# Kernel tuning notes

Hardware: AMD Instinct MI355X
Metric: run time of the kernel (lower is better)

Reference implementation:

```python
import jax, jax.numpy as jnp
import numpy as np

B, T, D, N, H = 1, 256, 512, 8, 64  # batch, seq, d_model, n_heads, d_head
INIT_STD = 0.02
IGNORE = -1000000.0
DUMMY_LOGIT = -1000.0


def setup_inputs() -> dict:
    key = jax.random.key(0)
    ks = jax.random.split(key, 9)
    std = INIT_STD
    inp = {
        'normalized_resid_pre': jax.random.normal(ks[0], (B, T, D), dtype=jnp.float32),
        'W_K1': jax.random.normal(ks[1], (N, D, H), dtype=jnp.float32) * std,
        'W_K2': jax.random.normal(ks[2], (N, D, H), dtype=jnp.float32) * std,
        'W_Q':  jax.random.normal(ks[3], (N, D, H), dtype=jnp.float32) * std,
        'W_V1': jax.random.normal(ks[4], (N, D, H), dtype=jnp.float32) * std,
        'W_V2': jax.random.normal(ks[5], (N, D, H), dtype=jnp.float32) * std,
        'W_Kq': jax.random.normal(ks[6], (N, H, H, H), dtype=jnp.float32) * std,
        'W_Vq': jax.random.normal(ks[7], (N, H, H, H), dtype=jnp.float32) * std,
        'W_O':  jax.random.normal(ks[8], (N, H, D), dtype=jnp.float32) * std,
        'b_K1': jnp.zeros((N, H), dtype=jnp.float32),
        'b_K2': jnp.zeros((N, H), dtype=jnp.float32),
        'b_Q':  jnp.zeros((N, H), dtype=jnp.float32),
        'b_V1': jnp.zeros((N, H), dtype=jnp.float32),
        'b_V2': jnp.zeros((N, H), dtype=jnp.float32),
        'b_O':  jnp.zeros((D,), dtype=jnp.float32),
    }
    return inp


def _trittention(x, W_K1, W_K2, W_Q, W_V1, W_V2, W_Kq, W_Vq, W_O,
                 b_K1, b_K2, b_Q, b_V1, b_V2, b_O):
    b, t, d = x.shape
    n, _, h = W_Q.shape
    proj = lambda W, bias: jnp.einsum('ndh,bpd->bpnh', W, x) + bias
    k1 = proj(W_K1, b_K1)  # (b, t, n, h)
    k2 = proj(W_K2, b_K2)
    q  = proj(W_Q,  b_Q)
    v1 = proj(W_V1, b_V1)
    v2 = proj(W_V2, b_V2)

    # bilinear value over pairs of positions: (b, n, h, s, t) -> flatten (s t)
    v = jnp.einsum('bsni,btnj,nijh->bnhst', v1, v2, W_Vq)
    v = v.reshape(b, n, h, t * t)

    # cubic scores: (b, n, s, t, r) with s=k1 pos, t=k2 pos, r=query pos
    step1 = jnp.einsum('brnk,nijk->bnrij', q, W_Kq)
    step2 = jnp.einsum('bnrij,btnj->bnrit', step1, k2)
    attn = jnp.einsum('bnrit,bsni->bnstr', step2, k1)

    # causal + ordering mask (order_attn=True, attn_eq=False):
    # masked if s>=r or t>=r or s>=t
    s_idx = jnp.arange(t)[:, None, None]
    t_idx = jnp.arange(t)[None, :, None]
    r_idx = jnp.arange(t)[None, None, :]
    mask = (s_idx >= r_idx) | (t_idx >= r_idx) | (s_idx >= t_idx)
    attn = jnp.where(mask, IGNORE, attn)

    # rearrange 'b n s t r -> b n r (s t)' and scale by d_head
    attn = jnp.transpose(attn, (0, 1, 4, 2, 3)).reshape(b, n, t, t * t) / h

    # causal_attn=True: append dummy logit / zero value slot
    dummy_logit = jnp.full((b, n, t, 1), DUMMY_LOGIT, dtype=attn.dtype)
    attn = jnp.concatenate([attn, dummy_logit], axis=-1)
    dummy_value = jnp.zeros((b, n, h, 1), dtype=v.dtype)
    v = jnp.concatenate([v, dummy_value], axis=-1)

    attn = jax.nn.softmax(attn, axis=-1)
    z = jnp.einsum('bnql,bnhl->bqnh', attn, v)
    out = jnp.einsum('bpnh,nhd->bpd', z, W_O) + b_O  # sum over heads folded in
    return out


def reference(normalized_resid_pre, W_K1, W_K2, W_Q, W_V1, W_V2, W_Kq, W_Vq, W_O,
              b_K1, b_K2, b_Q, b_V1, b_V2, b_O):
    return _trittention(normalized_resid_pre, W_K1, W_K2, W_Q, W_V1, W_V2,
                        W_Kq, W_Vq, W_O, b_K1, b_K2, b_Q, b_V1, b_V2, b_O)
```

## Files before the change

kernel.cpp:

```cpp
#include <hip/hip_runtime.h>
#include <hip/hip_bf16.h>
#include <math.h>

#define TT 256
#define DD 512
#define NN 8
#define HH 64
#define PROJ 131072

typedef __attribute__((ext_vector_type(8))) short short8v;
typedef __attribute__((ext_vector_type(4))) short short4v;
typedef __attribute__((ext_vector_type(4))) float f32x4;

__device__ __forceinline__ short f2bf(float x) {
    __hip_bfloat16 h = __float2bfloat16(x);
    return *reinterpret_cast<short*>(&h);
}

#define LGKM0 asm volatile("s_waitcnt lgkmcnt(0)" ::: "memory")

#define F_NUM  0
#define F_DEN  131072
#define F_END  133120
#define S_PB   0
#define S_XB   655360
#define S_WB   786432
#define S_KQB  2097152
#define S_VQB  4194304
#define S_WOB  6291456
#define S_S1B  6553600
#define S_AB   14942208
#define S_GB   23330816

__global__ __launch_bounds__(256) void prep_kernel(
    const float* __restrict__ x, const float* __restrict__ W_Kq,
    const float* __restrict__ W0, const float* __restrict__ W1,
    const float* __restrict__ W2, const float* __restrict__ W3,
    const float* __restrict__ W4, const float* __restrict__ Vq,
    const float* __restrict__ WO, short* __restrict__ sb, float* __restrict__ fz)
{
    __shared__ float plds[64 * 129];
    int b = blockIdx.x;
    int tid = threadIdx.x;
    if (b < 1024) {
        int i = b * 256 + tid;
        const float4 f0 = *(const float4*)(W_Kq + (size_t)i * 8);
        const float4 f1 = *(const float4*)(W_Kq + (size_t)i * 8 + 4);
        short8v o;
        o[0]=f2bf(f0.x); o[1]=f2bf(f0.y); o[2]=f2bf(f0.z); o[3]=f2bf(f0.w);
        o[4]=f2bf(f1.x); o[5]=f2bf(f1.y); o[6]=f2bf(f1.z); o[7]=f2bf(f1.w);
        *(short8v*)(sb + S_KQB + (size_t)i * 8) = o;
    } else if (b < 1088) {
        int i = (b - 1024) * 256 + tid;
        const float4 f0 = *(const float4*)(x + (size_t)i * 8);
        const float4 f1 = *(const float4*)(x + (size_t)i * 8 + 4);
        short8v o;
        o[0]=f2bf(f0.x); o[1]=f2bf(f0.y); o[2]=f2bf(f0.z); o[3]=f2bf(f0.w);
        o[4]=f2bf(f1.x); o[5]=f2bf(f1.y); o[6]=f2bf(f1.z); o[7]=f2bf(f1.w);
        *(short8v*)(sb + S_XB + (size_t)i * 8) = o;
    } else if (b < 1128) {
        int pn = b - 1088; int p = pn >> 3, n = pn & 7;
        const float* Wp = (p==0)?W0:(p==1)?W1:(p==2)?W2:(p==3)?W3:W4;
        const float* src = Wp + (size_t)n * DD * HH;
        short* dst = sb + S_WB + (size_t)pn * HH * DD;
        for (int d0 = 0; d0 < DD; d0 += 64) {
            __syncthreads();
            for (int it = 0; it < 16; ++it) {
                int m = it * 256 + tid;
                int dl = m >> 6, h = m & 63;
                plds[h * 65 + dl] = src[(size_t)(d0 + dl) * 64 + h];
            }
            __syncthreads();
            int h = tid >> 2, seg = tid & 3;
            short8v o0, o1;
            #pragma unroll
            for (int e = 0; e < 8; ++e) o0[e] = f2bf(plds[h * 65 + seg * 16 + e]);
            #pragma unroll
            for (int e = 0; e < 8; ++e) o1[e] = f2bf(plds[h * 65 + seg * 16 + 8 + e]);
            *(short8v*)(dst + (size_t)h * DD + d0 + seg * 16) = o0;
            *(short8v*)(dst + (size_t)h * DD + d0 + seg * 16 + 8) = o1;
        }
    } else if (b < 1640) {
        int bb = b - 1128; int n = bb >> 6, i = bb & 63;
        const float* src = Vq + (size_t)(n * 64 + i) * 4096;
        for (int it = 0; it < 16; ++it) {
            int m = it * 256 + tid;
            int j = m >> 6, h = m & 63;
            plds[h * 65 + j] = src[(size_t)j * 64 + h];
        }
        __syncthreads();
        int h = tid >> 2, seg = tid & 3;
        short8v o0, o1;
        #pragma unroll
        for (int e = 0; e < 8; ++e) o0[e] = f2bf(plds[h * 65 + seg * 16 + e]);
        #pragma unroll
        for (int e = 0; e < 8; ++e) o1[e] = f2bf(plds[h * 65 + seg * 16 + 8 + e]);
        short* dst = sb + S_VQB + (size_t)n * 262144 + (size_t)h * 4096 + i * 64 + seg * 16;
        *(short8v*)dst = o0;
        *(short8v*)(dst + 8) = o1;
    } else if (b < 1672) {
        int bb = b - 1640; int dc = bb & 7, nhc = bb >> 3;
        for (int it = 0; it < 32; ++it) {
            int m = it * 256 + tid;
            int nhl = m >> 6, dl = m & 63;
            plds[dl * 129 + nhl] = WO[(size_t)(nhc * 128 + nhl) * 512 + dc * 64 + dl];
        }
        __syncthreads();
        for (int it = 0; it < 4; ++it) {
            int m = it * 256 + tid;
            int dl = m >> 4, seg = m & 15;
            short8v o;
            #pragma unroll
            for (int e = 0; e < 8; ++e) o[e] = f2bf(plds[dl * 129 + seg * 8 + e]);
            *(short8v*)(sb + S_WOB + (size_t)(dc * 64 + dl) * 512 + nhc * 128 + seg * 8) = o;
        }
    } else {
        int i = (b - 1672) * 1024 + tid * 4;
        *(float4*)(fz + i) = make_float4(0.f, 0.f, 0.f, 0.f);
    }
}

__global__ __launch_bounds__(512) void proj_kernel(
    const short* __restrict__ xb, const short* __restrict__ Wb,
    const float* __restrict__ bK1, const float* __restrict__ bK2,
    const float* __restrict__ bQ,  const float* __restrict__ bV1,
    const float* __restrict__ bV2, short* __restrict__ Pb) {
    int p = blockIdx.x, n = blockIdx.y, mhalf = blockIdx.z;
    int wv = threadIdx.x >> 6, lane = threadIdx.x & 63, g = lane >> 4, c = lane & 15;
    __shared__ short wlds[64 * 520];
    __shared__ short sbuf[8][16 * 72];
    const short* wsrc = Wb + (size_t)(p * 8 + n) * HH * DD;
    for (int it = 0; it < 8; ++it) {
        int idx = it * 512 + threadIdx.x;
        int h = idx >> 6, seg = idx & 63;
        *(short8v*)(&wlds[h * 520 + seg * 8]) = *(const short8v*)(wsrc + (size_t)h * DD + seg * 8);
    }
    __syncthreads();
    int mt = mhalf * 8 + wv;
    f32x4 acc[4];
    #pragma unroll
    for (int ct = 0; ct < 4; ++ct) acc[ct] = (f32x4){0.f, 0.f, 0.f, 0.f};
    for (int ks = 0; ks < 16; ++ks) {
        short8v a = *(const short8v*)(xb + (size_t)(mt * 16 + c) * DD + ks * 32 + g * 8);
        #pragma unroll
        for (int ct = 0; ct < 4; ++ct) {
            short8v b = *(const short8v*)(&wlds[(ct * 16 + c) * 520 + ks * 32 + g * 8]);
            acc[ct] = __builtin_amdgcn_mfma_f32_16x16x32_bf16(a, b, acc[ct], 0, 0, 0);
        }
    }
    const float* bp = (p == 0) ? bK1 : (p == 1) ? bK2 : (p == 2) ? bQ : (p == 3) ? bV1 : bV2;
    short* sbw = &sbuf[wv][0];
    #pragma unroll
    for (int ct = 0; ct < 4; ++ct) {
        float bias = bp[n * 64 + ct * 16 + c];
        #pragma unroll
        for (int m = 0; m < 4; ++m)
            sbw[(g * 4 + m) * 72 + ct * 16 + c] = f2bf(acc[ct][m] + bias);
    }
    LGKM0;
    int rl = lane & 15, sg = lane >> 4;
    short8v o0 = *(const short8v*)(&sbw[rl * 72 + sg * 16]);
    short8v o1 = *(const short8v*)(&sbw[rl * 72 + sg * 16 + 8]);
    short* dst = Pb + (size_t)p * PROJ + (size_t)(n * 256 + mt * 16 + rl) * 64 + sg * 16;
    *(short8v*)dst = o0;
    *(short8v*)(dst + 8) = o1;
}

__global__ __launch_bounds__(256) void bgemm_kernel(
    const short* __restrict__ A0, const short* __restrict__ B0, short* __restrict__ O0,
    const short* __restrict__ A1, const short* __restrict__ B1, short* __restrict__ O1) {
    int mt = blockIdx.x, n = blockIdx.y, z = blockIdx.z;
    const short* A = (z < 4) ? A0 : A1;
    const short* B = (z < 4) ? B0 : B1;
    short* out = (z < 4) ? O0 : O1;
    int cgq = z & 3;
    int wv = threadIdx.x >> 6, lane = threadIdx.x & 63, g = lane >> 4, c = lane & 15;
    __shared__ short sbuf[4][16 * 72];
    short* sbw = &sbuf[wv][0];
    const short* abase = A + ((size_t)n * 256 + mt * 16 + c) * 64 + g * 8;
    short8v a0 = *(const short8v*)abase;
    short8v a1 = *(const short8v*)(abase + 32);
    for (int cg = cgq * 16 + wv; cg < cgq * 16 + 16; cg += 4) {
        f32x4 acc[4];
        #pragma unroll
        for (int jt = 0; jt < 4; ++jt) acc[jt] = (f32x4){0.f, 0.f, 0.f, 0.f};
        const short* bb = B + ((size_t)n * 4096 + cg * 64) * 64;
        #pragma unroll
        for (int jt = 0; jt < 4; ++jt) {
            short8v b0 = *(const short8v*)(bb + (size_t)(jt * 16 + c) * 64 + g * 8);
            short8v b1 = *(const short8v*)(bb + (size_t)(jt * 16 + c) * 64 + g * 8 + 32);
            acc[jt] = __builtin_amdgcn_mfma_f32_16x16x32_bf16(a0, b0, acc[jt], 0, 0, 0);
            acc[jt] = __builtin_amdgcn_mfma_f32_16x16x32_bf16(a1, b1, acc[jt], 0, 0, 0);
        }
        LGKM0;
        #pragma unroll
        for (int jt = 0; jt < 4; ++jt)
            #pragma unroll
            for (int m = 0; m < 4; ++m)
                sbw[(g * 4 + m) * 72 + jt * 16 + c] = f2bf(acc[jt][m]);
        LGKM0;
        int rl = lane & 15, sg = lane >> 4;
        short8v o0 = *(const short8v*)(&sbw[rl * 72 + sg * 16]);
        short8v o1 = *(const short8v*)(&sbw[rl * 72 + sg * 16 + 8]);
        short* dst = out + ((size_t)n * 256 + mt * 16 + rl) * 4096 + cg * 64 + sg * 16;
        *(short8v*)dst = o0;
        *(short8v*)(dst + 8) = o1;
    }
}

__global__ __launch_bounds__(256) void gmat_kernel(const short* __restrict__ S1b,
                                                   const short* __restrict__ K2b,
                                                   short* __restrict__ G) {
    int bid = blockIdx.x;
    int n = bid & 7;
    int tt = (bid >> 3) & 15;
    int rq = bid >> 7;
    int wv = threadIdx.x >> 6, lane = threadIdx.x & 63, g = lane >> 4, c = lane & 15;
    int t0 = tt * 16;
    __shared__ short sbuf[4][16 * 68];
    short* sbw = &sbuf[wv][0];
    const short* abase = K2b + ((size_t)n * TT + t0 + c) * 64 + g * 8;
    short8v a0 = *(const short8v*)abase;
    short8v a1 = *(const short8v*)(abase + 32);
    for (int r = t0 + rq * 4 + wv; r < 256; r += 16) {
        const short* bb = S1b + ((size_t)(n * 256 + r) * 64) * 64;
        f32x4 acc[4];
        #pragma unroll
        for (int it = 0; it < 4; ++it) {
            short8v b0 = *(const short8v*)(bb + (size_t)(it * 16 + c) * 64 + g * 8);
            short8v b1 = *(const short8v*)(bb + (size_t)(it * 16 + c) * 64 + g * 8 + 32);
            acc[it] = (f32x4){0.f, 0.f, 0.f, 0.f};
            acc[it] = __builtin_amdgcn_mfma_f32_16x16x32_bf16(a0, b0, acc[it], 0, 0, 0);
            acc[it] = __builtin_amdgcn_mfma_f32_16x16x32_bf16(a1, b1, acc[it], 0, 0, 0);
        }
        LGKM0;
        #pragma unroll
        for (int it = 0; it < 4; ++it)
            #pragma unroll
            for (int m = 0; m < 4; ++m)
                sbw[(g * 4 + m) * 68 + it * 16 + c] = f2bf(acc[it][m] * 0.015625f);
        LGKM0;
        int trow = lane >> 2, seg = (lane & 3) * 16;
        short8v o0 = *(const short8v*)(&sbw[trow * 68 + seg]);
        short8v o1 = *(const short8v*)(&sbw[trow * 68 + seg + 8]);
        short* dst = G + (((size_t)(n * TT + t0 + trow)) * TT + r) * 64 + seg;
        *(short8v*)dst = o0;
        *(short8v*)(dst + 8) = o1;
    }
}

__global__ __launch_bounds__(1024) void attn_kernel(
    const short* __restrict__ K1b, const short* __restrict__ V1b,
    const short* __restrict__ Gm, const short* __restrict__ Ab,
    float* __restrict__ num, float* __restrict__ den)
{
    int bid = blockIdx.x;
    int n = bid & 7;
    int rest = bid >> 3;
    int pair = rest >> 2;
    int sig = rest & 3;
    int tid = threadIdx.x;
    int wv = tid >> 6, lane = tid & 63, g = lane >> 4, c = lane & 15;

    __shared__ short k1lds[64 * 72];
    __shared__ short v1lds[64 * 72];
    __shared__ short u_lds[2][64 * 68];

    int t0H = (31 - pair) * 8;
    int stmaxK = (t0H + 6) >> 4;
    int cntK = (stmaxK >= sig) ? ((stmaxK - sig) >> 2) + 1 : 0;
    for (int idx = tid; idx < cntK * 128; idx += 1024) {
        int row = idx >> 3, seg = idx & 7;
        int s = (sig + (row >> 4) * 4) * 16 + (row & 15);
        *(short8v*)(&k1lds[row * 72 + seg * 8]) =
            *(const short8v*)(K1b + ((size_t)n * TT + s) * 64 + seg * 8);
        *(short8v*)(&v1lds[row * 72 + seg * 8]) =
            *(const short8v*)(V1b + ((size_t)n * TT + s) * 64 + seg * 8);
    }
    __syncthreads();

    f32x4 numacc[4];
    #pragma unroll
    for (int b = 0; b < 4; ++b) numacc[b] = (f32x4){0.f, 0.f, 0.f, 0.f};
    float denacc = 0.f;
    int rt = wv;
    int lU = wv >> 2, hU = wv & 3;
    int ubuf = 0;

    const short* vr = &v1lds[(lU * 16 + c) * 72 + g * 8];
    short8v vf0 = *(const short8v*)vr;
    short8v vf1 = *(const short8v*)(vr + 32);

    for (int part = 0; part < 2; ++part) {
        int t0 = part ? t0H : pair * 8;
        for (int th = 0; th < 8; ++th) {
            int t = t0 + th;
            if (t < 1 || t > 254) continue;
            int rt_start = (t + 1) >> 4;
            int stmaxU = (t - 1) >> 4;
            int cntU = (stmaxU >= sig) ? ((stmaxU - sig) >> 2) + 1 : 0;
            if (cntU == 0) continue;

            bool valid = (rt >= rt_start);
            short8v gf0, gf1;
            if (valid) {
                const short* gb = Gm + (((size_t)(n * TT + t) * TT) + rt * 16 + c) * 64 + g * 8;
                gf0 = *(const short8v*)gb;
                gf1 = *(const short8v*)(gb + 32);
            }

            short* uw = &u_lds[ubuf][0];
            if (lU < cntU) {
                const short* ar = Ab + (size_t)(n * TT + t) * 4096 + (hU * 16 + c) * 64 + g * 8;
                short8v ab0 = *(const short8v*)ar;
                short8v ab1 = *(const short8v*)(ar + 32);
                f32x4 ucc = (f32x4){0.f, 0.f, 0.f, 0.f};
                ucc = __builtin_amdgcn_mfma_f32_16x16x32_bf16(vf0, ab0, ucc, 0, 0, 0);
                ucc = __builtin_amdgcn_mfma_f32_16x16x32_bf16(vf1, ab1, ucc, 0, 0, 0);
                short4v uo;
                #pragma unroll
                for (int m = 0; m < 4; ++m) uo[m] = f2bf(ucc[m]);
                *(short4v*)(&uw[(hU * 16 + c) * 68 + lU * 16 + g * 4]) = uo;
            }
            __syncthreads();
            ubuf ^= 1;

            if (valid) {
                int r = rt * 16 + c;
                for (int loc = 0; loc < cntU; ++loc) {
                    int s_base = (sig + loc * 4) * 16;
                    const short* kr = &k1lds[(loc * 16 + c) * 72 + g * 8];
                    short8v af0 = *(const short8v*)kr;
                    short8v af1 = *(const short8v*)(kr + 32);
                    f32x4 lg = (f32x4){0.f, 0.f, 0.f, 0.f};
                    lg = __builtin_amdgcn_mfma_f32_16x16x32_bf16(af0, gf0, lg, 0, 0, 0);
                    lg = __builtin_amdgcn_mfma_f32_16x16x32_bf16(af1, gf1, lg, 0, 0, 0);
                    short4v eb;
                    float dsum = 0.f;
                    #pragma unroll
                    for (int m = 0; m < 4; ++m) {
                        int s = s_base + g * 4 + m;
                        float e = (s < t && r > t) ? __expf(lg[m]) : 0.f;
                        dsum += e;
                        eb[m] = f2bf(e);
                    }
                    denacc += dsum;
                    #pragma unroll
                    for (int hs = 0; hs < 4; ++hs) {
                        short4v ub = *(const short4v*)(&uw[(hs * 16 + c) * 68 + loc * 16 + g * 4]);
                        numacc[hs] = __builtin_amdgcn_mfma_f32_16x16x16bf16_1k(eb, ub, numacc[hs], 0, 0, 0);
                    }
                }
            }
        }
    }

    if (__any(denacc != 0.f)) {
        float v = denacc;
        v += __shfl_xor(v, 16);
        v += __shfl_xor(v, 32);
        if (lane < 16) atomicAdd(&den[n * TT + rt * 16 + lane], v);
        #pragma unroll
        for (int hs = 0; hs < 4; ++hs)
            #pragma unroll
            for (int m = 0; m < 4; ++m)
                atomicAdd(&num[((size_t)(n * TT + rt * 16 + g * 4 + m)) * 64 + hs * 16 + c],
                          numacc[hs][m]);
    }
}

__global__ __launch_bounds__(512) void out_kernel(const float* __restrict__ num,
                                                  const float* __restrict__ den,
                                                  const short* __restrict__ WOb,
                                                  const float* __restrict__ bO,
                                                  float* __restrict__ out) {
    int mt = blockIdx.x & 15, dq = blockIdx.x >> 4;
    int wv = threadIdx.x >> 6, lane = threadIdx.x & 63, g = lane >> 4, c = lane & 15;
    int dt0 = dq * 16 + wv * 2;
    int t = mt * 16 + c;
    f32x4 acc[2];
    acc[0] = (f32x4){0.f, 0.f, 0.f, 0.f};
    acc[1] = (f32x4){0.f, 0.f, 0.f, 0.f};
    for (int ks = 0; ks < 16; ++ks) {
        int nh = ks * 32 + g * 8;
        int nn = nh >> 6, h = nh & 63;
        float dv = den[nn * 256 + t];
        float rcp = (dv > 0.f) ? 1.f / dv : 0.f;
        const float* np = num + ((size_t)(nn * 256 + t) * 64 + h);
        float4 f0 = *(const float4*)np;
        float4 f1 = *(const float4*)(np + 4);
        short8v a;
        a[0]=f2bf(f0.x*rcp); a[1]=f2bf(f0.y*rcp); a[2]=f2bf(f0.z*rcp); a[3]=f2bf(f0.w*rcp);
        a[4]=f2bf(f1.x*rcp); a[5]=f2bf(f1.y*rcp); a[6]=f2bf(f1.z*rcp); a[7]=f2bf(f1.w*rcp);
        #pragma unroll
        for (int u = 0; u < 2; ++u) {
            short8v b = *(const short8v*)(WOb + (size_t)((dt0 + u) * 16 + c) * 512 + ks * 32 + g * 8);
            acc[u] = __builtin_amdgcn_mfma_f32_16x16x32_bf16(a, b, acc[u], 0, 0, 0);
        }
    }
    #pragma unroll
    for (int u = 0; u < 2; ++u) {
        int d = (dt0 + u) * 16 + c;
        float bias = bO[d];
        #pragma unroll
        for (int m = 0; m < 4; ++m)
            out[(size_t)(mt * 16 + g * 4 + m) * 512 + d] = acc[u][m] + bias;
    }
}

extern "C" void kernel_launch(void* const* d_in, const int* in_sizes, int n_in,
                              void* d_out, int out_size, void* d_ws, size_t ws_size,
                              hipStream_t stream) {
    const float* x    = (const float*)d_in[0];
    const float* W_K1 = (const float*)d_in[1];
    const float* W_K2 = (const float*)d_in[2];
    const float* W_Q  = (const float*)d_in[3];
    const float* W_V1 = (const float*)d_in[4];
    const float* W_V2 = (const float*)d_in[5];
    const float* W_Kq = (const float*)d_in[6];
    const float* W_Vq = (const float*)d_in[7];
    const float* W_O  = (const float*)d_in[8];
    const float* b_K1 = (const float*)d_in[9];
    const float* b_K2 = (const float*)d_in[10];
    const float* b_Q  = (const float*)d_in[11];
    const float* b_V1 = (const float*)d_in[12];
    const float* b_V2 = (const float*)d_in[13];
    const float* b_O  = (const float*)d_in[14];
    float* ws = (float*)d_ws;
    short* sb = (short*)(ws + F_END);
    float* out = (float*)d_out;

    prep_kernel<<<1802, 256, 0, stream>>>(x, W_Kq, W_K1, W_K2, W_Q, W_V1, W_V2,
                                          W_Vq, W_O, sb, ws + F_NUM);

    proj_kernel<<<dim3(5, 8, 2), 512, 0, stream>>>(sb + S_XB, sb + S_WB,
                                                   b_K1, b_K2, b_Q, b_V1, b_V2, sb + S_PB);

    bgemm_kernel<<<dim3(16, 8, 8), 256, 0, stream>>>(
        sb + S_PB + 2 * PROJ, sb + S_KQB, sb + S_S1B,
        sb + S_PB + 4 * PROJ, sb + S_VQB, sb + S_AB);

    gmat_kernel<<<512, 256, 0, stream>>>(sb + S_S1B, sb + S_PB + 1 * PROJ, sb + S_GB);

    attn_kernel<<<512, 1024, 0, stream>>>(sb + S_PB, sb + S_PB + 3 * PROJ,
                                          sb + S_GB, sb + S_AB,
                                          ws + F_NUM, ws + F_DEN);

    out_kernel<<<32, 512, 0, stream>>>(ws + F_NUM, ws + F_DEN, sb + S_WOB, b_O, out);
}
```

Before: 142.9 us.

## Repartition attention work: 2-way s-interleave with 4-step paired t chunks per block

Changes the attn_kernel work split from 4-way s-tile interleave with 8-step t chunks to 2-way s interleave with 4-step low/high paired t chunks, keeping the grid-size relationship implied by bid decoding. Each block now holds up to 8 s-tiles of K1/V1 in LDS and each wave computes two U tiles per t, doubling LDS buffers. The aim is better load balance across blocks and more MFMA work per sync. The cost is more LDS use and per-wave registers, which may reduce occupancy, and each block's atomics cover fewer t values. The host launch grid must match the new block decoding.

```diff
diff --git a/kernel.cpp b/kernel.cpp
--- a/kernel.cpp
+++ b/kernel.cpp
@@ -256,22 +256,21 @@
 {
     int bid = blockIdx.x;
     int n = bid & 7;
-    int rest = bid >> 3;
-    int pair = rest >> 2;
-    int sig = rest & 3;
+    int sig = (bid >> 3) & 1;
+    int q = bid >> 4;
     int tid = threadIdx.x;
     int wv = tid >> 6, lane = tid & 63, g = lane >> 4, c = lane & 15;
 
-    __shared__ short k1lds[64 * 72];
-    __shared__ short v1lds[64 * 72];
-    __shared__ short u_lds[2][64 * 68];
-
-    int t0H = (31 - pair) * 8;
-    int stmaxK = (t0H + 6) >> 4;
-    int cntK = (stmaxK >= sig) ? ((stmaxK - sig) >> 2) + 1 : 0;
+    __shared__ short k1lds[128 * 72];
+    __shared__ short v1lds[128 * 72];
+    __shared__ short u_lds[2][64 * 136];
+
+    int t0L = q * 4, t0H = (63 - q) * 4;
+    int stmaxK = (t0H + 2) >> 4;
+    int cntK = (stmaxK >= sig) ? ((stmaxK - sig) >> 1) + 1 : 0;
     for (int idx = tid; idx < cntK * 128; idx += 1024) {
         int row = idx >> 3, seg = idx & 7;
-        int s = (sig + (row >> 4) * 4) * 16 + (row & 15);
+        int s = (sig + (row >> 4) * 2) * 16 + (row & 15);
         *(short8v*)(&k1lds[row * 72 + seg * 8]) =
             *(const short8v*)(K1b + ((size_t)n * TT + s) * 64 + seg * 8);
         *(short8v*)(&v1lds[row * 72 + seg * 8]) =
@@ -285,71 +284,77 @@
     float denacc = 0.f;
     int rt = wv;
     int lU = wv >> 2, hU = wv & 3;
-    int ubuf = 0;
-
-    const short* vr = &v1lds[(lU * 16 + c) * 72 + g * 8];
-    short8v vf0 = *(const short8v*)vr;
-    short8v vf1 = *(const short8v*)(vr + 32);
-
-    for (int part = 0; part < 2; ++part) {
-        int t0 = part ? t0H : pair * 8;
-        for (int th = 0; th < 8; ++th) {
-            int t = t0 + th;
-            if (t < 1 || t > 254) continue;
-            int rt_start = (t + 1) >> 4;
-            int stmaxU = (t - 1) >> 4;
-            int cntU = (stmaxU >= sig) ? ((stmaxU - sig) >> 2) + 1 : 0;
-            if (cntU == 0) continue;
-
-            bool valid = (rt >= rt_start);
-            short8v gf0, gf1;
-            if (valid) {
-                const short* gb = Gm + (((size_t)(n * TT + t) * TT) + rt * 16 + c) * 64 + g * 8;
-                gf0 = *(const short8v*)gb;
-                gf1 = *(const short8v*)(gb + 32);
-            }
-
-            short* uw = &u_lds[ubuf][0];
-            if (lU < cntU) {
-                const short* ar = Ab + (size_t)(n * TT + t) * 4096 + (hU * 16 + c) * 64 + g * 8;
-                short8v ab0 = *(const short8v*)ar;
-                short8v ab1 = *(const short8v*)(ar + 32);
-                f32x4 ucc = (f32x4){0.f, 0.f, 0.f, 0.f};
-                ucc = __builtin_amdgcn_mfma_f32_16x16x32_bf16(vf0, ab0, ucc, 0, 0, 0);
-                ucc = __builtin_amdgcn_mfma_f32_16x16x32_bf16(vf1, ab1, ucc, 0, 0, 0);
+
+    const short* vrpA = &v1lds[(lU * 16 + c) * 72 + g * 8];
+    short8v vfA0 = *(const short8v*)vrpA;
+    short8v vfA1 = *(const short8v*)(vrpA + 32);
+    const short* vrpB = &v1lds[((lU + 4) * 16 + c) * 72 + g * 8];
+    short8v vfB0 = *(const short8v*)vrpB;
+    short8v vfB1 = *(const short8v*)(vrpB + 32);
+
+    for (int i = 0; i < 8; ++i) {
+        int t = (i < 4) ? (t0L + i) : (t0H + i - 4);
+        int stmaxU = (t - 1) >> 4;
+        int cntU = (t >= 1 && t <= 254 && stmaxU >= sig) ? ((stmaxU - sig) >> 1) + 1 : 0;
+
+        bool valid = cntU && (rt >= ((t + 1) >> 4));
+        short8v gf0, gf1;
+        if (valid) {
+            const short* gb = Gm + (((size_t)(n * TT + t) * TT) + rt * 16 + c) * 64 + g * 8;
+            gf0 = *(const short8v*)gb;
+            gf1 = *(const short8v*)(gb + 32);
+        }
+
+        short* uw = &u_lds[i & 1][0];
+        if (cntU && lU < cntU) {
+            const short* ar = Ab + (size_t)(n * TT + t) * 4096 + (hU * 16 + c) * 64 + g * 8;
+            short8v ab0 = *(const short8v*)ar;
+            short8v ab1 = *(const short8v*)(ar + 32);
+            {
+                f32x4 u = (f32x4){0.f, 0.f, 0.f, 0.f};
+                u = __builtin_amdgcn_mfma_f32_16x16x32_bf16(vfA0, ab0, u, 0, 0, 0);
+                u = __builtin_amdgcn_mfma_f32_16x16x32_bf16(vfA1, ab1, u, 0, 0, 0);
                 short4v uo;
                 #pragma unroll
-                for (int m = 0; m < 4; ++m) uo[m] = f2bf(ucc[m]);
-                *(short4v*)(&uw[(hU * 16 + c) * 68 + lU * 16 + g * 4]) = uo;
+                for (int m = 0; m < 4; ++m) uo[m] = f2bf(u[m]);
+                *(short4v*)(&uw[(hU * 16 + c) * 136 + lU * 16 + g * 4]) = uo;
             }
-            __syncthreads();
-            ubuf ^= 1;
-
-            if (valid) {
-                int r = rt * 16 + c;
-                for (int loc = 0; loc < cntU; ++loc) {
-                    int s_base = (sig + loc * 4) * 16;
-                    const short* kr = &k1lds[(loc * 16 + c) * 72 + g * 8];
-                    short8v af0 = *(const short8v*)kr;
-                    short8v af1 = *(const short8v*)(kr + 32);
-                    f32x4 lg = (f32x4){0.f, 0.f, 0.f, 0.f};
-                    lg = __builtin_amdgcn_mfma_f32_16x16x32_bf16(af0, gf0, lg, 0, 0, 0);
-                    lg = __builtin_amdgcn_mfma_f32_16x16x32_bf16(af1, gf1, lg, 0, 0, 0);
-                    short4v eb;
-                    float dsum = 0.f;
-                    #pragma unroll
-                    for (int m = 0; m < 4; ++m) {
-                        int s = s_base + g * 4 + m;
-                        float e = (s < t && r > t) ? __expf(lg[m]) : 0.f;
-                        dsum += e;
-                        eb[m] = f2bf(e);
-                    }
-                    denacc += dsum;
-                    #pragma unroll
-                    for (int hs = 0; hs < 4; ++hs) {
-                        short4v ub = *(const short4v*)(&uw[(hs * 16 + c) * 68 + loc * 16 + g * 4]);
-                        numacc[hs] = __builtin_amdgcn_mfma_f32_16x16x16bf16_1k(eb, ub, numacc[hs], 0, 0, 0);
-                    }
+            if (lU + 4 < cntU) {
+                f32x4 u = (f32x4){0.f, 0.f, 0.f, 0.f};
+                u = __builtin_amdgcn_mfma_f32_16x16x32_bf16(vfB0, ab0, u, 0, 0, 0);
+                u = __builtin_amdgcn_mfma_f32_16x16x32_bf16(vfB1, ab1, u, 0, 0, 0);
+                short4v uo;
+                #pragma unroll
+                for (int m = 0; m < 4; ++m) uo[m] = f2bf(u[m]);
+                *(short4v*)(&uw[(hU * 16 + c) * 136 + (lU + 4) * 16 + g * 4]) = uo;
+            }
+        }
+        __syncthreads();
+
+        if (valid) {
+            int r = rt * 16 + c;
+            for (int loc = 0; loc < cntU; ++loc) {
+                int s_base = (sig + loc * 2) * 16;
+                const short* kr = &k1lds[(loc * 16 + c) * 72 + g * 8];
+                short8v af0 = *(const short8v*)kr;
+                short8v af1 = *(const short8v*)(kr + 32);
+                f32x4 lg = (f32x4){0.f, 0.f, 0.f, 0.f};
+                lg = __builtin_amdgcn_mfma_f32_16x16x32_bf16(af0, gf0, lg, 0, 0, 0);
+                lg = __builtin_amdgcn_mfma_f32_16x16x32_bf16(af1, gf1, lg, 0, 0, 0);
+                short4v eb;
+                float dsum = 0.f;
+                #pragma unroll
+                for (int m = 0; m < 4; ++m) {
+                    int s = s_base + g * 4 + m;
+                    float e = (s < t && r > t) ? __expf(lg[m]) : 0.f;
+                    dsum += e;
+                    eb[m] = f2bf(e);
+                }
+                denacc += dsum;
+                #pragma unroll
+                for (int hs = 0; hs < 4; ++hs) {
+                    short4v ub = *(const short4v*)(&uw[(hs * 16 + c) * 136 + loc * 16 + g * 4]);
+                    numacc[hs] = __builtin_amdgcn_mfma_f32_16x16x16bf16_1k(eb, ub, numacc[hs], 0, 0, 0);
                 }
             }
         }
```

Result: no change. 142.2 us (-0.4%).

## Repartition attention kernel by query tile and remove per-step block barriers

Applied to the files above, without the earlier changes.

The attention kernel's work split changes. Each block now owns one 16-row query tile of one head and strides over t positions across its 8 waves, instead of grouping blocks by t-pair and s-stripe. Each wave now computes the U = V1·A tile itself in registers, which removes the shared U buffer and the __syncthreads on every t step. The cost is that the U MFMA work is repeated for every query tile, and the load is uneven because low query tiles cover few t values.

```diff
diff --git a/kernel.cpp b/kernel.cpp
--- a/kernel.cpp
+++ b/kernel.cpp
@@ -249,33 +249,32 @@
     }
 }
 
-__global__ __launch_bounds__(1024) void attn_kernel(
+__global__ __launch_bounds__(512) void attn_kernel(
     const short* __restrict__ K1b, const short* __restrict__ V1b,
     const short* __restrict__ Gm, const short* __restrict__ Ab,
     float* __restrict__ num, float* __restrict__ den)
 {
     int bid = blockIdx.x;
     int n = bid & 7;
-    int rest = bid >> 3;
-    int pair = rest >> 2;
-    int sig = rest & 3;
+    int rt = (bid >> 3) & 15;
+    int tq = bid >> 7;
     int tid = threadIdx.x;
     int wv = tid >> 6, lane = tid & 63, g = lane >> 4, c = lane & 15;
 
-    __shared__ short k1lds[64 * 72];
-    __shared__ short v1lds[64 * 72];
-    __shared__ short u_lds[2][64 * 68];
-
-    int t0H = (31 - pair) * 8;
-    int stmaxK = (t0H + 6) >> 4;
-    int cntK = (stmaxK >= sig) ? ((stmaxK - sig) >> 2) + 1 : 0;
-    for (int idx = tid; idx < cntK * 128; idx += 1024) {
+    __shared__ short k1lds[256 * 72];
+    __shared__ short v1lds[256 * 72];
+
+    int tmax = rt * 16 + 14;
+    if (tmax > 254) tmax = 254;
+    int rows = (rt + 1) * 16;
+    if (rows > 256) rows = 256;
+
+    for (int idx = tid; idx < rows * 8; idx += 512) {
         int row = idx >> 3, seg = idx & 7;
-        int s = (sig + (row >> 4) * 4) * 16 + (row & 15);
         *(short8v*)(&k1lds[row * 72 + seg * 8]) =
-            *(const short8v*)(K1b + ((size_t)n * TT + s) * 64 + seg * 8);
+            *(const short8v*)(K1b + ((size_t)n * TT + row) * 64 + seg * 8);
         *(short8v*)(&v1lds[row * 72 + seg * 8]) =
-            *(const short8v*)(V1b + ((size_t)n * TT + s) * 64 + seg * 8);
+            *(const short8v*)(V1b + ((size_t)n * TT + row) * 64 + seg * 8);
     }
     __syncthreads();
 
@@ -283,75 +282,56 @@
     #pragma unroll
     for (int b = 0; b < 4; ++b) numacc[b] = (f32x4){0.f, 0.f, 0.f, 0.f};
     float denacc = 0.f;
-    int rt = wv;
-    int lU = wv >> 2, hU = wv & 3;
-    int ubuf = 0;
-
-    const short* vr = &v1lds[(lU * 16 + c) * 72 + g * 8];
-    short8v vf0 = *(const short8v*)vr;
-    short8v vf1 = *(const short8v*)(vr + 32);
-
-    for (int part = 0; part < 2; ++part) {
-        int t0 = part ? t0H : pair * 8;
-        for (int th = 0; th < 8; ++th) {
-            int t = t0 + th;
-            if (t < 1 || t > 254) continue;
-            int rt_start = (t + 1) >> 4;
-            int stmaxU = (t - 1) >> 4;
-            int cntU = (stmaxU >= sig) ? ((stmaxU - sig) >> 2) + 1 : 0;
-            if (cntU == 0) continue;
-
-            bool valid = (rt >= rt_start);
-            short8v gf0, gf1;
-            if (valid) {
-                const short* gb = Gm + (((size_t)(n * TT + t) * TT) + rt * 16 + c) * 64 + g * 8;
-                gf0 = *(const short8v*)gb;
-                gf1 = *(const short8v*)(gb + 32);
+    int r = rt * 16 + c;
+
+    for (int t = tq + 8 * wv; t <= tmax; t += 64) {
+        if (t < 1) continue;
+        int cntU = ((t - 1) >> 4) + 1;
+
+        short8v ab0[4], ab1[4];
+        #pragma unroll
+        for (int hs = 0; hs < 4; ++hs) {
+            const short* ar = Ab + (size_t)(n * TT + t) * 4096 + (hs * 16 + c) * 64 + g * 8;
+            ab0[hs] = *(const short8v*)ar;
+            ab1[hs] = *(const short8v*)(ar + 32);
+        }
+        const short* gb = Gm + (((size_t)(n * TT + t) * TT) + rt * 16 + c) * 64 + g * 8;
+        short8v gf0 = *(const short8v*)gb;
+        short8v gf1 = *(const short8v*)(gb + 32);
+
+        for (int loc = 0; loc < cntU; ++loc) {
+            const short* vr = &v1lds[(loc * 16 + c) * 72 + g * 8];
+            short8v vf0 = *(const short8v*)vr;
+            short8v vf1 = *(const short8v*)(vr + 32);
+            short4v ub[4];
+            #pragma unroll
+            for (int hs = 0; hs < 4; ++hs) {
+                f32x4 u = (f32x4){0.f, 0.f, 0.f, 0.f};
+                u = __builtin_amdgcn_mfma_f32_16x16x32_bf16(vf0, ab0[hs], u, 0, 0, 0);
+                u = __builtin_amdgcn_mfma_f32_16x16x32_bf16(vf1, ab1[hs], u, 0, 0, 0);
+                #pragma unroll
+                for (int m = 0; m < 4; ++m) ub[hs][m] = f2bf(u[m]);
             }
-
-            short* uw = &u_lds[ubuf][0];
-            if (lU < cntU) {
-                const short* ar = Ab + (size_t)(n * TT + t) * 4096 + (hU * 16 + c) * 64 + g * 8;
-                short8v ab0 = *(const short8v*)ar;
-                short8v ab1 = *(const short8v*)(ar + 32);
-                f32x4 ucc = (f32x4){0.f, 0.f, 0.f, 0.f};
-                ucc = __builtin_amdgcn_mfma_f32_16x16x32_bf16(vf0, ab0, ucc, 0, 0, 0);
-                ucc = __builtin_amdgcn_mfma_f32_16x16x32_bf16(vf1, ab1, ucc, 0, 0, 0);
-                short4v uo;
-                #pragma unroll
-                for (int m = 0; m < 4; ++m) uo[m] = f2bf(ucc[m]);
-                *(short4v*)(&uw[(hU * 16 + c) * 68 + lU * 16 + g * 4]) = uo;
+            const short* kr = &k1lds[(loc * 16 + c) * 72 + g * 8];
+            short8v af0 = *(const short8v*)kr;
+            short8v af1 = *(const short8v*)(kr + 32);
+            f32x4 lg = (f32x4){0.f, 0.f, 0.f, 0.f};
+            lg = __builtin_amdgcn_mfma_f32_16x16x32_bf16(af0, gf0, lg, 0, 0, 0);
+            lg = __builtin_amdgcn_mfma_f32_16x16x32_bf16(af1, gf1, lg, 0, 0, 0);
+            int s_base = loc * 16;
+            short4v eb;
+            float dsum = 0.f;
+            #pragma unroll
+            for (int m = 0; m < 4; ++m) {
+                int s = s_base + g * 4 + m;
+                float e = (s < t && r > t) ? __expf(lg[m]) : 0.f;
+                dsum += e;
+                eb[m] = f2bf(e);
             }
-            __syncthreads();
-            ubuf ^= 1;
-
-            if (valid) {
-                int r = rt * 16 + c;
-                for (int loc = 0; loc < cntU; ++loc) {
-                    int s_base = (sig + loc * 4) * 16;
-                    const short* kr = &k1lds[(loc * 16 + c) * 72 + g * 8];
-                    short8v af0 = *(const short8v*)kr;
-                    short8v af1 = *(const short8v*)(kr + 32);
-                    f32x4 lg = (f32x4){0.f, 0.f, 0.f, 0.f};
-                    lg = __builtin_amdgcn_mfma_f32_16x16x32_bf16(af0, gf0, lg, 0, 0, 0);
-                    lg = __builtin_amdgcn_mfma_f32_16x16x32_bf16(af1, gf1, lg, 0, 0, 0);
-                    short4v eb;
-                    float dsum = 0.f;
-                    #pragma unroll
-                    for (int m = 0; m < 4; ++m) {
-                        int s = s_base + g * 4 + m;
-                        float e = (s < t && r > t) ? __expf(lg[m]) : 0.f;
-                        dsum += e;
-                        eb[m] = f2bf(e);
-                    }
-                    denacc += dsum;
-                    #pragma unroll
-                    for (int hs = 0; hs < 4; ++hs) {
-                        short4v ub = *(const short4v*)(&uw[(hs * 16 + c) * 68 + loc * 16 + g * 4]);
-                        numacc[hs] = __builtin_amdgcn_mfma_f32_16x16x16bf16_1k(eb, ub, numacc[hs], 0, 0, 0);
-                    }
-                }
-            }
+            denacc += dsum;
+            #pragma unroll
+            for (int hs = 0; hs < 4; ++hs)
+                numacc[hs] = __builtin_amdgcn_mfma_f32_16x16x16bf16_1k(eb, ub[hs], numacc[hs], 0, 0, 0);
         }
     }
 
@@ -442,7 +422,7 @@
 
     gmat_kernel<<<512, 256, 0, stream>>>(sb + S_S1B, sb + S_PB + 1 * PROJ, sb + S_GB);
 
-    attn_kernel<<<512, 1024, 0, stream>>>(sb + S_PB, sb + S_PB + 3 * PROJ,
+    attn_kernel<<<1024, 512, 0, stream>>>(sb + S_PB, sb + S_PB + 3 * PROJ,
                                           sb + S_GB, sb + S_AB,
                                           ws + F_NUM, ws + F_DEN);
 
```

New measurement: 143.7 us. No clear change (+0.6%).
